# Kernel optimization log

Measured on AMD Instinct MI355X. Metric: run time of the kernel, lower is better.

## Reference

```python
import jax, jax.numpy as jnp
import numpy as np

EPS = 1e-6
GROUPS = 8


def setup_inputs() -> dict:
    key = jax.random.key(0)
    ks = jax.random.split(key, 8)
    B, C, H, W = 4, 128, 64, 64
    s = 1.0 / np.sqrt(C)
    return {
        "x": jax.random.normal(ks[0], (B, C, H, W), jnp.float32),
        "gn_scale": jnp.ones((C,), jnp.float32),
        "gn_bias": jnp.zeros((C,), jnp.float32),
        "wq": jax.random.normal(ks[1], (C, C), jnp.float32) * s,
        "bq": jnp.zeros((C,), jnp.float32),
        "wk": jax.random.normal(ks[2], (C, C), jnp.float32) * s,
        "bk": jnp.zeros((C,), jnp.float32),
        "wv": jax.random.normal(ks[3], (C, C), jnp.float32) * s,
        "bv": jnp.zeros((C,), jnp.float32),
        "wp": jax.random.normal(ks[4], (C, C), jnp.float32) * s,
        "bp": jnp.zeros((C,), jnp.float32),
    }


def _group_norm(x, scale, bias):
    B, C, H, W = x.shape
    g = x.reshape(B, GROUPS, C // GROUPS, H * W)
    mu = g.mean(axis=(2, 3), keepdims=True)
    var = g.var(axis=(2, 3), keepdims=True)
    g = (g - mu) * jax.lax.rsqrt(var + EPS)
    g = g.reshape(B, C, H, W)
    return g * scale[None, :, None, None] + bias[None, :, None, None]


def reference(x, gn_scale, gn_bias, wq, bq, wk, bk, wv, bv, wp, bp):
    B, C, H, W = x.shape
    N = H * W
    h = _group_norm(x, gn_scale, gn_bias).reshape(B, C, N)
    # 1x1 convs == channel matmuls: (C_out, C_in) x (B, C_in, N)
    q = jnp.einsum('oc,bcn->bon', wq, h) + bq[None, :, None]
    k = jnp.einsum('oc,bcn->bon', wk, h) + bk[None, :, None]
    v = jnp.einsum('oc,bcn->bon', wv, h) + bv[None, :, None]
    # scores: (B, N, N), w[b,n,m] = sum_c q[b,c,n] k[b,c,m]
    w = jnp.einsum('bcn,bcm->bnm', q, k) * (C ** -0.5)
    w = jax.nn.softmax(w, axis=-1)
    # h_[b,c,n] = sum_m w[b,n,m] v[b,c,m]
    h_ = jnp.einsum('bnm,bcm->bcn', w, v)
    out = jnp.einsum('oc,bcn->bon', wp, h_) + bp[None, :, None]
    return x + out.reshape(B, C, H, W)
```

## Files before the change

### kernel.cpp

```cpp
#include <hip/hip_runtime.h>
#include <math.h>

#define B_ 4
#define C_ 128
#define N_ 4096
#define NSPLIT 4
#define MT 32
#define PLD 40
#define HLD 136
#define VTLD 24

typedef float floatx4 __attribute__((ext_vector_type(4)));
typedef short bf16x8 __attribute__((ext_vector_type(8)));

__device__ __forceinline__ ushort f2bf(float f) {
  unsigned u = __float_as_uint(f);
  return (ushort)((u + 0x7FFF + ((u >> 16) & 1)) >> 16);
}
__device__ __forceinline__ float bf2f(ushort u) {
  return __uint_as_float(((unsigned)u) << 16);
}
__device__ __forceinline__ unsigned pkbf(float a, float b) {
  return __builtin_amdgcn_perm(__float_as_uint(a) + 0x8000u,
                               __float_as_uint(b) + 0x8000u, 0x07060302u);
}
__device__ __forceinline__ void gl2lds16(const ushort* g, ushort* l) {
  __builtin_amdgcn_global_load_lds(
      (const __attribute__((address_space(1))) void*)g,
      (__attribute__((address_space(3))) void*)l, 16, 0, 0);
}

__global__ __launch_bounds__(256) void prep_kernel(
    const float* __restrict__ x, float* __restrict__ gstat,
    const float* __restrict__ wq, const float* __restrict__ wk,
    const float* __restrict__ wv, const float* __restrict__ wp,
    ushort* __restrict__ wB) {
  if (blockIdx.x >= 256) {
    int i = (blockIdx.x - 256) * 256 + threadIdx.x;
    int m = i >> 14, j = i & 16383;
    const float* src = (m == 0) ? wq : (m == 1) ? wk : (m == 2) ? wv : wp;
    wB[i] = f2bf(src[j]);
    return;
  }
  int b = blockIdx.x >> 6, g = (blockIdx.x >> 3) & 7, part = blockIdx.x & 7;
  const float4* xp = (const float4*)(x + (size_t)(b * C_ + g * 16) * N_) + part * 2048;
  float s = 0.f, ss = 0.f;
  for (int i = threadIdx.x; i < 2048; i += 256) {
    float4 v = xp[i];
    s += v.x + v.y + v.z + v.w;
    ss += v.x * v.x + v.y * v.y + v.z * v.z + v.w * v.w;
  }
  #pragma unroll
  for (int o = 32; o > 0; o >>= 1) {
    s += __shfl_down(s, o, 64);
    ss += __shfl_down(ss, o, 64);
  }
  __shared__ float rs[4], rss[4];
  int wid = threadIdx.x >> 6, lane = threadIdx.x & 63;
  if (lane == 0) { rs[wid] = s; rss[wid] = ss; }
  __syncthreads();
  if (threadIdx.x == 0) {
    int slot = (b * 8 + g) * 8 + part;
    gstat[slot]       = rs[0] + rs[1] + rs[2] + rs[3];
    gstat[256 + slot] = rss[0] + rss[1] + rss[2] + rss[3];
  }
}

__global__ __launch_bounds__(256) void gnqkv_kernel(
    const float* __restrict__ x, const float* __restrict__ gstat,
    const float* __restrict__ scale, const float* __restrict__ bias,
    const ushort* __restrict__ wB,
    const float* __restrict__ bq, const float* __restrict__ bk,
    const float* __restrict__ bv,
    ushort* __restrict__ qT, ushort* __restrict__ kT, ushort* __restrict__ vB) {
  __shared__ __align__(16) ushort hs[16][HLD];
  __shared__ __align__(16) ushort Qt[16][HLD];
  __shared__ __align__(16) ushort Kt[16][HLD];
  __shared__ __align__(16) ushort Vt[128][VTLD];
  __shared__ float sSc[C_], sBi[C_];
  int tid = threadIdx.x;
  int b = blockIdx.x >> 8;
  int n0 = (blockIdx.x & 255) * 16;
  if (tid < 128) {
    int g = tid >> 4;
    float S = 0.f, SS = 0.f;
    #pragma unroll
    for (int p = 0; p < 8; ++p) {
      S  += gstat[(b * 8 + g) * 8 + p];
      SS += gstat[256 + (b * 8 + g) * 8 + p];
    }
    float mu = S * (1.f / 65536.f);
    float var = SS * (1.f / 65536.f) - mu * mu;
    float rstd = rsqrtf(var + 1e-6f);
    float sc = scale[tid] * rstd;
    sSc[tid] = sc;
    sBi[tid] = bias[tid] - mu * sc;
  }
  __syncthreads();
  #pragma unroll
  for (int k2 = 0; k2 < 2; ++k2) {
    int i = tid + k2 * 256;
    int c = i >> 2, n4 = i & 3;
    float4 v = *(const float4*)(x + (size_t)(b * C_ + c) * N_ + n0 + n4 * 4);
    float sc = sSc[c], bi = sBi[c];
    hs[n4 * 4 + 0][c] = f2bf(v.x * sc + bi);
    hs[n4 * 4 + 1][c] = f2bf(v.y * sc + bi);
    hs[n4 * 4 + 2][c] = f2bf(v.z * sc + bi);
    hs[n4 * 4 + 3][c] = f2bf(v.w * sc + bi);
  }
  __syncthreads();
  int lane = tid & 63, w = tid >> 6;
  int col = lane & 15, quad = lane >> 4;
  int oh = w * 32;
  bf16x8 hf[4];
  #pragma unroll
  for (int kc = 0; kc < 4; ++kc)
    hf[kc] = *(const bf16x8*)&hs[col][kc * 32 + quad * 8];
  const ushort* Wq = wB;
  const ushort* Wk = wB + 16384;
  const ushort* Wv = wB + 32768;
  const float scl = 0.12751879752224991f;
  #pragma unroll
  for (int ot = 0; ot < 2; ++ot) {
    int o0 = oh + ot * 16;
    floatx4 aq = (floatx4)0.f, ak = (floatx4)0.f, av = (floatx4)0.f;
    #pragma unroll
    for (int kc = 0; kc < 4; ++kc) {
      int wo = (o0 + col) * C_ + kc * 32 + quad * 8;
      aq = __builtin_amdgcn_mfma_f32_16x16x32_bf16(*(const bf16x8*)&Wq[wo], hf[kc], aq, 0, 0, 0);
      ak = __builtin_amdgcn_mfma_f32_16x16x32_bf16(*(const bf16x8*)&Wk[wo], hf[kc], ak, 0, 0, 0);
      av = __builtin_amdgcn_mfma_f32_16x16x32_bf16(*(const bf16x8*)&Wv[wo], hf[kc], av, 0, 0, 0);
    }
    float4 bqv = *(const float4*)&bq[o0 + quad * 4];
    float4 bkv = *(const float4*)&bk[o0 + quad * 4];
    float4 bvv = *(const float4*)&bv[o0 + quad * 4];
    uint2 qs = { pkbf((aq[1] + bqv.y) * scl, (aq[0] + bqv.x) * scl),
                 pkbf((aq[3] + bqv.w) * scl, (aq[2] + bqv.z) * scl) };
    uint2 ks = { pkbf(ak[1] + bkv.y, ak[0] + bkv.x),
                 pkbf(ak[3] + bkv.w, ak[2] + bkv.z) };
    *(uint2*)&Qt[col][o0 + quad * 4] = qs;
    *(uint2*)&Kt[col][o0 + quad * 4] = ks;
    float vv[4] = {av[0] + bvv.x, av[1] + bvv.y, av[2] + bvv.z, av[3] + bvv.w};
    #pragma unroll
    for (int r = 0; r < 4; ++r)
      Vt[o0 + quad * 4 + r][col] = f2bf(vv[r]);
  }
  __syncthreads();
  {
    int row = tid >> 4, seg = tid & 15;
    size_t dst = ((size_t)b * N_ + n0 + row) * C_ + seg * 8;
    *(uint4*)(qT + dst) = *(const uint4*)&Qt[row][seg * 8];
    *(uint4*)(kT + dst) = *(const uint4*)&Kt[row][seg * 8];
  }
  {
    int o = tid >> 1, seg = tid & 1;
    *(uint4*)(vB + ((size_t)b * C_ + o) * N_ + n0 + seg * 8) = *(const uint4*)&Vt[o][seg * 8];
  }
}

__global__ __launch_bounds__(512, 4) void attn_kernel(
    const ushort* __restrict__ qT, const ushort* __restrict__ kT,
    const ushort* __restrict__ vB, ushort* __restrict__ Op,
    float* __restrict__ Lv) {
  __shared__ __align__(16) ushort Ks[2][MT * 128];
  __shared__ __align__(16) ushort Vs[2][C_ * MT];
  __shared__ __align__(16) ushort Ps[128 * PLD];
  __shared__ float lpart[8][2][16];
  int sp = blockIdx.x & 3;
  int qblk = (blockIdx.x >> 2) & 31;
  int b = blockIdx.x >> 7;
  int n0 = qblk * 128;
  int tid = threadIdx.x, lane = tid & 63, w = tid >> 6;
  int col = lane & 15, quad = lane >> 4;
  int wu = __builtin_amdgcn_readfirstlane(w);
  int mtw = w & 1, qg = w >> 1;
  int qh = w & 1, cq = w >> 1;
  const ushort* kTb = kT + (size_t)b * N_ * C_;
  const ushort* vBb = vB + (size_t)b * C_ * N_;

  bf16x8 qf[2][4];
  #pragma unroll
  for (int qt = 0; qt < 2; ++qt)
    #pragma unroll
    for (int kc = 0; kc < 4; ++kc)
      qf[qt][kc] = *(const bf16x8*)(qT + ((size_t)b * N_ + n0 + qg * 32 + qt * 16 + col) * C_ + kc * 32 + quad * 8);

  floatx4 Oacc[4][2];
  #pragma unroll
  for (int qt = 0; qt < 4; ++qt)
    #pragma unroll
    for (int ct = 0; ct < 2; ++ct) Oacc[qt][ct] = (floatx4)0.f;
  float lacc[2] = {0.f, 0.f};

  #define STAGE(m0v, buf)                                                            \
    {                                                                                \
      int r = wu * 4 + (lane >> 4);                                                  \
      int pos = (lane & 15) ^ (r & 7);                                               \
      gl2lds16(kTb + (size_t)((m0v) + r) * 128 + pos * 8, &Ks[buf][wu * 512]);       \
      int c = wu * 16 + (lane >> 2);                                                 \
      gl2lds16(vBb + (size_t)c * N_ + (m0v) + (lane & 3) * 8, &Vs[buf][wu * 512]);   \
    }

  STAGE(sp * 1024, 0);
  __syncthreads();

  for (int it = 0; it < 1024 / MT; ++it) {
    if (it < 1024 / MT - 1) STAGE(sp * 1024 + (it + 1) * MT, (it + 1) & 1);
    const ushort* KsB = Ks[it & 1];
    const ushort* VsB = Vs[it & 1];

    floatx4 st[2];
    {
      int row = mtw * 16 + col;
      bf16x8 kf[4];
      #pragma unroll
      for (int kc = 0; kc < 4; ++kc)
        kf[kc] = *(const bf16x8*)&KsB[row * 128 + (((4 * kc + quad) ^ (col & 7)) * 8)];
      #pragma unroll
      for (int qt = 0; qt < 2; ++qt) {
        floatx4 acc = (floatx4)0.f;
        #pragma unroll
        for (int kc = 0; kc < 4; ++kc)
          acc = __builtin_amdgcn_mfma_f32_16x16x32_bf16(kf[kc], qf[qt][kc], acc, 0, 0, 0);
        st[qt] = acc;
      }
    }
    #pragma unroll
    for (int qt = 0; qt < 2; ++qt) {
      int prow = (qg * 32 + qt * 16 + col) * PLD + mtw * 16;
      float p0 = exp2f(st[qt][0]);
      float p1 = exp2f(st[qt][1]);
      float p2 = exp2f(st[qt][2]);
      float p3 = exp2f(st[qt][3]);
      uint2 pk = { pkbf(p1, p0), pkbf(p3, p2) };
      *(uint2*)&Ps[prow + quad * 4] = pk;
      lacc[qt] += (p0 + p1) + (p2 + p3);
    }
    __syncthreads();
    bf16x8 vf[2];
    #pragma unroll
    for (int ct = 0; ct < 2; ++ct)
      vf[ct] = *(const bf16x8*)&VsB[(cq * 32 + ct * 16 + col) * MT + quad * 8];
    #pragma unroll
    for (int qt = 0; qt < 4; ++qt) {
      bf16x8 pf = *(const bf16x8*)&Ps[(qh * 64 + qt * 16 + col) * PLD + quad * 8];
      #pragma unroll
      for (int ct = 0; ct < 2; ++ct)
        Oacc[qt][ct] = __builtin_amdgcn_mfma_f32_16x16x32_bf16(pf, vf[ct], Oacc[qt][ct], 0, 0, 0);
    }
    __syncthreads();
  }

  ushort* OpB = Op + (((size_t)sp * B_ + b) * N_ + n0) * C_;
  #pragma unroll
  for (int qt = 0; qt < 4; ++qt)
    #pragma unroll
    for (int ct = 0; ct < 2; ++ct)
      #pragma unroll
      for (int r = 0; r < 4; ++r)
        OpB[(size_t)(qh * 64 + qt * 16 + quad * 4 + r) * C_ + cq * 32 + ct * 16 + col] =
            f2bf(Oacc[qt][ct][r]);
  #pragma unroll
  for (int qt = 0; qt < 2; ++qt) {
    float lsum = lacc[qt];
    lsum += __shfl_xor(lsum, 16, 64);
    lsum += __shfl_xor(lsum, 32, 64);
    if (quad == 0) lpart[w][qt][col] = lsum;
  }
  __syncthreads();
  if ((w & 1) == 0 && quad == 0) {
    #pragma unroll
    for (int qt = 0; qt < 2; ++qt) {
      int idx = b * N_ + n0 + (w >> 1) * 32 + qt * 16 + col;
      Lv[(size_t)sp * (B_ * N_) + idx] = lpart[w][qt][col] + lpart[w + 1][qt][col];
    }
  }
}

__global__ __launch_bounds__(256) void mergeproj_kernel(
    const ushort* __restrict__ Op, const float* __restrict__ Lv,
    const ushort* __restrict__ wpB, const float* __restrict__ bp,
    const float* __restrict__ x, float* __restrict__ out) {
  __shared__ __align__(16) ushort tile[16 * HLD];
  int tid = threadIdx.x;
  int b = blockIdx.x >> 8;
  int n0 = (blockIdx.x & 255) * 16;
  {
    int n = tid >> 4, cc = tid & 15;
    int nIdx = b * N_ + n0 + n;
    float den = Lv[0 * (B_ * N_) + nIdx] + Lv[1 * (B_ * N_) + nIdx] +
                Lv[2 * (B_ * N_) + nIdx] + Lv[3 * (B_ * N_) + nIdx];
    float inv = 1.f / den;
    float o[8];
    #pragma unroll
    for (int j = 0; j < 8; ++j) o[j] = 0.f;
    #pragma unroll
    for (int sp = 0; sp < NSPLIT; ++sp) {
      uint4 d = *(const uint4*)&Op[((size_t)sp * (B_ * N_) + nIdx) * C_ + cc * 8];
      unsigned dd[4] = {d.x, d.y, d.z, d.w};
      #pragma unroll
      for (int j = 0; j < 4; ++j) {
        o[j * 2]     += bf2f((ushort)(dd[j] & 0xFFFF));
        o[j * 2 + 1] += bf2f((ushort)(dd[j] >> 16));
      }
    }
    uint4 res;
    res.x = pkbf(o[1] * inv, o[0] * inv);
    res.y = pkbf(o[3] * inv, o[2] * inv);
    res.z = pkbf(o[5] * inv, o[4] * inv);
    res.w = pkbf(o[7] * inv, o[6] * inv);
    *(uint4*)&tile[n * HLD + cc * 8] = res;
  }
  __syncthreads();
  int lane = tid & 63, w = tid >> 6;
  int col = lane & 15, quad = lane >> 4;
  int oh = w * 32;
  bf16x8 hf[4];
  #pragma unroll
  for (int kc = 0; kc < 4; ++kc)
    hf[kc] = *(const bf16x8*)&tile[col * HLD + kc * 32 + quad * 8];
  #pragma unroll
  for (int ot = 0; ot < 2; ++ot) {
    int o0 = oh + ot * 16;
    floatx4 acc = (floatx4)0.f;
    #pragma unroll
    for (int kc = 0; kc < 4; ++kc) {
      int wo = (o0 + col) * C_ + kc * 32 + quad * 8;
      acc = __builtin_amdgcn_mfma_f32_16x16x32_bf16(*(const bf16x8*)&wpB[wo], hf[kc], acc, 0, 0, 0);
    }
    float4 bpv = *(const float4*)&bp[o0 + quad * 4];
    float bb[4] = {bpv.x, bpv.y, bpv.z, bpv.w};
    #pragma unroll
    for (int r = 0; r < 4; ++r) {
      size_t idx = ((size_t)b * C_ + o0 + quad * 4 + r) * N_ + n0 + col;
      out[idx] = acc[r] + bb[r] + x[idx];
    }
  }
}

extern "C" void kernel_launch(void* const* d_in, const int* in_sizes, int n_in,
                              void* d_out, int out_size, void* d_ws, size_t ws_size,
                              hipStream_t stream) {
  const float* x        = (const float*)d_in[0];
  const float* gn_scale = (const float*)d_in[1];
  const float* gn_bias  = (const float*)d_in[2];
  const float* wq = (const float*)d_in[3];
  const float* bq = (const float*)d_in[4];
  const float* wk = (const float*)d_in[5];
  const float* bk = (const float*)d_in[6];
  const float* wv = (const float*)d_in[7];
  const float* bv = (const float*)d_in[8];
  const float* wp = (const float*)d_in[9];
  const float* bp = (const float*)d_in[10];
  float* out = (float*)d_out;

  char* ws = (char*)d_ws;
  float*  Lv    = (float*)(ws + 262144);
  ushort* wB    = (ushort*)(ws + 524288);
  float*  gstat = (float*)(ws + 655360);
  ushort* qT    = (ushort*)(ws + (4u << 20));
  ushort* kT    = (ushort*)(ws + (8u << 20));
  ushort* vB    = (ushort*)(ws + (12u << 20));
  ushort* Op    = (ushort*)(ws + (16u << 20));
  ushort* wpB   = wB + 49152;

  prep_kernel<<<512, 256, 0, stream>>>(x, gstat, wq, wk, wv, wp, wB);
  gnqkv_kernel<<<1024, 256, 0, stream>>>(x, gstat, gn_scale, gn_bias, wB, bq, bk, bv, qT, kT, vB);
  attn_kernel<<<512, 512, 0, stream>>>(qT, kT, vB, Op, Lv);
  mergeproj_kernel<<<1024, 256, 0, stream>>>(Op, Lv, wpB, bp, x, out);
}
```

Before: 154.8 us.

## Software-pipeline QK and PV stages with double-buffered P and a single barrier

Restructures the attention main loop so the S=QK^T MFMAs for tile t overlap with the PV MFMAs for tile t-1. P is double-buffered in shared memory and V fragments are loaded ahead, which removes one of the two barriers per iteration. It also XOR-swizzles the V staging layout to reduce LDS bank conflicts and raises wave priority around the MFMA blocks with s_setprio. The cost is more LDS for the second P buffer, more live registers, and a prologue and epilogue that must stay consistent with the staging buffers.

```diff
diff --git a/kernel.cpp b/kernel.cpp
--- a/kernel.cpp
+++ b/kernel.cpp
@@ -164,7 +164,7 @@
     float* __restrict__ Lv) {
   __shared__ __align__(16) ushort Ks[2][MT * 128];
   __shared__ __align__(16) ushort Vs[2][C_ * MT];
-  __shared__ __align__(16) ushort Ps[128 * PLD];
+  __shared__ __align__(16) ushort Ps[2][128 * PLD];
   __shared__ float lpart[8][2][16];
   int sp = blockIdx.x & 3;
   int qblk = (blockIdx.x >> 2) & 31;
@@ -198,58 +198,94 @@
       int pos = (lane & 15) ^ (r & 7);                                               \
       gl2lds16(kTb + (size_t)((m0v) + r) * 128 + pos * 8, &Ks[buf][wu * 512]);       \
       int c = wu * 16 + (lane >> 2);                                                 \
-      gl2lds16(vBb + (size_t)c * N_ + (m0v) + (lane & 3) * 8, &Vs[buf][wu * 512]);   \
-    }
-
-  STAGE(sp * 1024, 0);
-  __syncthreads();
-
-  for (int it = 0; it < 1024 / MT; ++it) {
-    if (it < 1024 / MT - 1) STAGE(sp * 1024 + (it + 1) * MT, (it + 1) & 1);
-    const ushort* KsB = Ks[it & 1];
-    const ushort* VsB = Vs[it & 1];
-
-    floatx4 st[2];
-    {
-      int row = mtw * 16 + col;
-      bf16x8 kf[4];
-      #pragma unroll
-      for (int kc = 0; kc < 4; ++kc)
-        kf[kc] = *(const bf16x8*)&KsB[row * 128 + (((4 * kc + quad) ^ (col & 7)) * 8)];
-      #pragma unroll
-      for (int qt = 0; qt < 2; ++qt) {
-        floatx4 acc = (floatx4)0.f;
-        #pragma unroll
-        for (int kc = 0; kc < 4; ++kc)
-          acc = __builtin_amdgcn_mfma_f32_16x16x32_bf16(kf[kc], qf[qt][kc], acc, 0, 0, 0);
-        st[qt] = acc;
-      }
-    }
-    #pragma unroll
-    for (int qt = 0; qt < 2; ++qt) {
-      int prow = (qg * 32 + qt * 16 + col) * PLD + mtw * 16;
-      float p0 = exp2f(st[qt][0]);
-      float p1 = exp2f(st[qt][1]);
-      float p2 = exp2f(st[qt][2]);
-      float p3 = exp2f(st[qt][3]);
-      uint2 pk = { pkbf(p1, p0), pkbf(p3, p2) };
-      *(uint2*)&Ps[prow + quad * 4] = pk;
-      lacc[qt] += (p0 + p1) + (p2 + p3);
-    }
+      int mc = (lane & 3) ^ ((lane >> 3) & 3);                                       \
+      gl2lds16(vBb + (size_t)c * N_ + (m0v) + mc * 8, &Vs[buf][wu * 512]);           \
+    }
+
+  #define S_COMPUTE(KsB, st)                                                          \
+    {                                                                                 \
+      int row = mtw * 16 + col;                                                       \
+      bf16x8 kf[4];                                                                   \
+      _Pragma("unroll")                                                               \
+      for (int kc = 0; kc < 4; ++kc)                                                  \
+        kf[kc] = *(const bf16x8*)&(KsB)[row * 128 + (((4 * kc + quad) ^ (col & 7)) * 8)]; \
+      __builtin_amdgcn_s_setprio(1);                                                  \
+      _Pragma("unroll")                                                               \
+      for (int qt = 0; qt < 2; ++qt) {                                                \
+        floatx4 acc = (floatx4)0.f;                                                   \
+        _Pragma("unroll")                                                             \
+        for (int kc = 0; kc < 4; ++kc)                                                \
+          acc = __builtin_amdgcn_mfma_f32_16x16x32_bf16(kf[kc], qf[qt][kc], acc, 0, 0, 0); \
+        st[qt] = acc;                                                                 \
+      }                                                                               \
+      __builtin_amdgcn_s_setprio(0);                                                  \
+    }
+
+  #define SOFTMAX_WRITE(PsB, st)                                                      \
+    {                                                                                 \
+      _Pragma("unroll")                                                               \
+      for (int qt = 0; qt < 2; ++qt) {                                                \
+        int prow = (qg * 32 + qt * 16 + col) * PLD + mtw * 16;                        \
+        float p0 = exp2f(st[qt][0]);                                                  \
+        float p1 = exp2f(st[qt][1]);                                                  \
+        float p2 = exp2f(st[qt][2]);                                                  \
+        float p3 = exp2f(st[qt][3]);                                                  \
+        uint2 pk = { pkbf(p1, p0), pkbf(p3, p2) };                                    \
+        *(uint2*)&(PsB)[prow + quad * 4] = pk;                                        \
+        lacc[qt] += (p0 + p1) + (p2 + p3);                                            \
+      }                                                                               \
+    }
+
+  #define V_LOAD(VsB, vfp)                                                            \
+    {                                                                                 \
+      _Pragma("unroll")                                                               \
+      for (int ct = 0; ct < 2; ++ct)                                                  \
+        vfp[ct] = *(const bf16x8*)&(VsB)[(cq * 32 + ct * 16 + col) * MT +             \
+                                         ((quad ^ ((col >> 1) & 3)) * 8)];            \
+    }
+
+  #define PV_COMPUTE(PsB, vfp)                                                        \
+    {                                                                                 \
+      __builtin_amdgcn_s_setprio(1);                                                  \
+      _Pragma("unroll")                                                               \
+      for (int qt = 0; qt < 4; ++qt) {                                                \
+        bf16x8 pf = *(const bf16x8*)&(PsB)[(qh * 64 + qt * 16 + col) * PLD + quad * 8]; \
+        _Pragma("unroll")                                                             \
+        for (int ct = 0; ct < 2; ++ct)                                                \
+          Oacc[qt][ct] = __builtin_amdgcn_mfma_f32_16x16x32_bf16(pf, vfp[ct], Oacc[qt][ct], 0, 0, 0); \
+      }                                                                               \
+      __builtin_amdgcn_s_setprio(0);                                                  \
+    }
+
+  const int m00 = sp * 1024;
+  floatx4 st[2];
+  bf16x8 vfp[2];
+
+  STAGE(m00, 0);
+  __syncthreads();
+
+  STAGE(m00 + MT, 1);
+  S_COMPUTE(Ks[0], st);
+  SOFTMAX_WRITE(Ps[0], st);
+  V_LOAD(Vs[0], vfp);
+  __syncthreads();
+
+  for (int t = 1; t < 31; ++t) {
+    STAGE(m00 + (t + 1) * MT, (t + 1) & 1);
+    S_COMPUTE(Ks[t & 1], st);
+    PV_COMPUTE(Ps[(t - 1) & 1], vfp);
+    SOFTMAX_WRITE(Ps[t & 1], st);
+    V_LOAD(Vs[t & 1], vfp);
     __syncthreads();
-    bf16x8 vf[2];
-    #pragma unroll
-    for (int ct = 0; ct < 2; ++ct)
-      vf[ct] = *(const bf16x8*)&VsB[(cq * 32 + ct * 16 + col) * MT + quad * 8];
-    #pragma unroll
-    for (int qt = 0; qt < 4; ++qt) {
-      bf16x8 pf = *(const bf16x8*)&Ps[(qh * 64 + qt * 16 + col) * PLD + quad * 8];
-      #pragma unroll
-      for (int ct = 0; ct < 2; ++ct)
-        Oacc[qt][ct] = __builtin_amdgcn_mfma_f32_16x16x32_bf16(pf, vf[ct], Oacc[qt][ct], 0, 0, 0);
-    }
-    __syncthreads();
-  }
+  }
+
+  S_COMPUTE(Ks[1], st);
+  PV_COMPUTE(Ps[0], vfp);
+  SOFTMAX_WRITE(Ps[1], st);
+  V_LOAD(Vs[1], vfp);
+  __syncthreads();
+
+  PV_COMPUTE(Ps[1], vfp);
 
   ushort* OpB = Op + (((size_t)sp * B_ + b) * N_ + n0) * C_;
   #pragma unroll
```

Result: no change. 155.4 us (+0.4%).
